# Performance work log

Measured on AMD Instinct MI355X. Metric: run time of the kernel, lower is better.

The kernel has to match this reference:

```python
import jax, jax.numpy as jnp
import numpy as np

B, N, D, H, K = 8, 128, 256, 128, 8

def setup_inputs() -> dict:
    key = jax.random.key(0)
    ks = jax.random.split(key, 6)
    E = jax.random.normal(ks[0], (B, N, D), dtype=jnp.float32)
    # kaiming_uniform-like init for linear weights
    lim1 = np.sqrt(6.0 / (2 * D))
    W1 = jax.random.uniform(ks[1], (H, 2 * D), minval=-lim1, maxval=lim1, dtype=jnp.float32)
    b1 = jnp.zeros((H,), dtype=jnp.float32)
    lim2 = np.sqrt(6.0 / H)
    W2 = jax.random.uniform(ks[2], (D, H), minval=-lim2, maxval=lim2, dtype=jnp.float32)
    b2 = jnp.zeros((D,), dtype=jnp.float32)
    q = jax.random.normal(ks[3], (K, D), dtype=jnp.float32) * (1.0 / D ** 0.5)
    return {"E": E, "W1": W1, "b1": b1, "W2": W2, "b2": b2, "q": q}

def reference(E, W1, b1, W2, b2, q):
    # phi(cat(Ei,Ej)) == relu(E_i @ W1a^T + E_j @ W1b^T + b1) @ W2^T + b2
    # Split first linear's weight to avoid materializing the [B,N,N,2D] concat.
    W1a, W1b = W1[:, :D], W1[:, D:]          # each [H, D]
    Ai = jnp.einsum('bnd,hd->bnh', E, W1a)   # [B,N,H] (row half)
    Aj = jnp.einsum('bnd,hd->bnh', E, W1b)   # [B,N,H] (col half)
    hidden = jax.nn.relu(Ai[:, :, None, :] + Aj[:, None, :, :] + b1)  # [B,N,N,H]
    # dropout is identity at inference
    # Fuse second linear with query dot: (hidden @ W2^T + b2) . q_h
    #   = hidden @ (W2^T q_h) + b2.q_h
    Wq = jnp.einsum('dh,kd->hk', W2, q)      # [H, K]
    bq = jnp.einsum('d,kd->k', b2, q)        # [K]
    logits = jnp.einsum('bijh,hk->bijh'[:0] or 'bijh,hk->bijk', hidden, Wq) + bq  # [B,N,N,K]
    M = jax.nn.sigmoid(logits).transpose(0, 3, 1, 2)  # [B,K,N,N]
    eye = jnp.eye(N, dtype=M.dtype)[None, None]
    return M * (1.0 - eye)
```

## Files before the change

kernel.cpp:

```cpp
#include <hip/hip_runtime.h>

#define PB 8
#define PN 128
#define PD 256
#define PH 128
#define PK 8
#define D2 (2*PD)

__global__ __launch_bounds__(256) void k0_prep(
        const float* __restrict__ W1, const float* __restrict__ W2,
        const float* __restrict__ b2, const float* __restrict__ q,
        float4* __restrict__ W1t4, float* __restrict__ Wq, float* __restrict__ bq)
{
    const int blk = blockIdx.x, t = threadIdx.x;
    if (blk < 64) {
        __shared__ float sm[32][33];
        const int h0 = (blk >> 4) * 32;
        const int d0 = (blk & 15) * 32;
        const int tx = t & 31, ty = t >> 5;
        #pragma unroll
        for (int r = 0; r < 4; ++r)
            sm[ty + 8 * r][tx] = W1[(h0 + ty + 8 * r) * D2 + d0 + tx];
        __syncthreads();
        const int hl = t & 31, dql = t >> 5;
        float4 w = make_float4(sm[hl][dql * 4 + 0], sm[hl][dql * 4 + 1],
                               sm[hl][dql * 4 + 2], sm[hl][dql * 4 + 3]);
        W1t4[((d0 >> 2) + dql) * PH + h0 + hl] = w;
    } else {
        __shared__ float qs[PD];
        __shared__ float red[256];
        const int k = blk - 64;
        qs[t] = q[k * PD + t];
        __syncthreads();
        if (t < PH) {
            float acc = 0.f;
            #pragma unroll 4
            for (int d = 0; d < PD; ++d)
                acc = fmaf(W2[d * PH + t], qs[d], acc);
            Wq[t * PK + k] = acc;
        }
        red[t] = b2[t] * qs[t];
        __syncthreads();
        for (int st = 128; st > 0; st >>= 1) {
            if (t < st) red[t] += red[t + st];
            __syncthreads();
        }
        if (t == 0) bq[k] = red[0];
    }
}

__global__ __launch_bounds__(256) void k1_proj(
        const float* __restrict__ E, const float* __restrict__ b1,
        const float4* __restrict__ W1t4,
        float* __restrict__ Ai, float* __restrict__ Ajt)
{
    const int blk = blockIdx.x, t = threadIdx.x;
    const int b    = blk >> 6;
    const int part = (blk >> 5) & 1;
    const int rg   = blk & 31;
    const int h    = t & (PH - 1);
    const int s    = t >> 7;
    const int n    = rg * 4 + 2 * s;

    const int ebase = __builtin_amdgcn_readfirstlane((b * PN + n) * PD);
    const float* e0 = E + ebase;
    const float* e1 = e0 + PD;
    const float4* wp = W1t4 + (part * 64) * PH + h;

    float a0 = 0.f, a1 = 0.f;
    #pragma unroll 8
    for (int dq = 0; dq < 64; ++dq) {
        const float4 w  = wp[dq * PH];
        const float4 p0 = *reinterpret_cast<const float4*>(e0 + dq * 4);
        const float4 p1 = *reinterpret_cast<const float4*>(e1 + dq * 4);
        a0 = fmaf(w.x, p0.x, a0); a0 = fmaf(w.y, p0.y, a0);
        a0 = fmaf(w.z, p0.z, a0); a0 = fmaf(w.w, p0.w, a0);
        a1 = fmaf(w.x, p1.x, a1); a1 = fmaf(w.y, p1.y, a1);
        a1 = fmaf(w.z, p1.z, a1); a1 = fmaf(w.w, p1.w, a1);
    }

    if (part == 0) {
        const float bb = b1[h];
        Ai[(b * PN + n + 0) * PH + h] = a0 + bb;
        Ai[(b * PN + n + 1) * PH + h] = a1 + bb;
    } else {
        *reinterpret_cast<float2*>(&Ajt[(b * PH + h) * PN + n]) =
            make_float2(a0, a1);
    }
}

__global__ __launch_bounds__(256) void k2_score(
        const float* __restrict__ Ai, const float* __restrict__ Ajt,
        const float4* __restrict__ Wq4, const float* __restrict__ bq,
        float* __restrict__ out)
{
    const int blk = blockIdx.x, t = threadIdx.x;
    const int b  = blk >> 5;
    const int i0 = (blk & 31) * 4;
    const int il = t >> 6;
    const int jb = t & 63;
    const int i  = i0 + il;

    const int aib = __builtin_amdgcn_readfirstlane((b * PN + i) * PH);
    const float* ai = Ai + aib;
    const float* aj = Ajt + b * PH * PN + jb;

    float acc0[PK], acc1[PK];
    const float q0 = bq[0], q1 = bq[1], q2 = bq[2], q3 = bq[3];
    const float q4 = bq[4], q5 = bq[5], q6 = bq[6], q7 = bq[7];
    acc0[0]=q0; acc0[1]=q1; acc0[2]=q2; acc0[3]=q3;
    acc0[4]=q4; acc0[5]=q5; acc0[6]=q6; acc0[7]=q7;
    acc1[0]=q0; acc1[1]=q1; acc1[2]=q2; acc1[3]=q3;
    acc1[4]=q4; acc1[5]=q5; acc1[6]=q6; acc1[7]=q7;

    #pragma unroll 8
    for (int hh = 0; hh < PH; ++hh) {
        const float a  = ai[hh];
        const float g0 = aj[hh * PN];
        const float g1 = aj[hh * PN + 64];
        const float v0 = fmaxf(a + g0, 0.f);
        const float v1 = fmaxf(a + g1, 0.f);
        const float4 wA = Wq4[hh * 2];
        const float4 wB = Wq4[hh * 2 + 1];
        acc0[0] = fmaf(v0, wA.x, acc0[0]); acc0[1] = fmaf(v0, wA.y, acc0[1]);
        acc0[2] = fmaf(v0, wA.z, acc0[2]); acc0[3] = fmaf(v0, wA.w, acc0[3]);
        acc0[4] = fmaf(v0, wB.x, acc0[4]); acc0[5] = fmaf(v0, wB.y, acc0[5]);
        acc0[6] = fmaf(v0, wB.z, acc0[6]); acc0[7] = fmaf(v0, wB.w, acc0[7]);
        acc1[0] = fmaf(v1, wA.x, acc1[0]); acc1[1] = fmaf(v1, wA.y, acc1[1]);
        acc1[2] = fmaf(v1, wA.z, acc1[2]); acc1[3] = fmaf(v1, wA.w, acc1[3]);
        acc1[4] = fmaf(v1, wB.x, acc1[4]); acc1[5] = fmaf(v1, wB.y, acc1[5]);
        acc1[6] = fmaf(v1, wB.z, acc1[6]); acc1[7] = fmaf(v1, wB.w, acc1[7]);
    }

    #pragma unroll
    for (int k = 0; k < PK; ++k) {
        float s0 = 1.f / (1.f + __expf(-acc0[k]));
        float s1 = 1.f / (1.f + __expf(-acc1[k]));
        if (jb == i)      s0 = 0.f;
        if (jb + 64 == i) s1 = 0.f;
        float* orow = out + ((b * PK + k) * PN + i) * PN;
        orow[jb]      = s0;
        orow[jb + 64] = s1;
    }
}

extern "C" void kernel_launch(void* const* d_in, const int* in_sizes, int n_in,
                              void* d_out, int out_size, void* d_ws, size_t ws_size,
                              hipStream_t stream) {
    const float* E  = (const float*)d_in[0];
    const float* W1 = (const float*)d_in[1];
    const float* b1 = (const float*)d_in[2];
    const float* W2 = (const float*)d_in[3];
    const float* b2 = (const float*)d_in[4];
    const float* q  = (const float*)d_in[5];

    float*  Ai   = (float*)d_ws;
    float*  Ajt  = Ai + PB * PN * PH;
    float4* W1t4 = (float4*)(Ajt + PB * PH * PN);
    float*  Wq   = (float*)(W1t4 + 128 * PH);
    float*  bq   = Wq + PH * PK;

    k0_prep<<<72,  256, 0, stream>>>(W1, W2, b2, q, W1t4, Wq, bq);
    k1_proj<<<512, 256, 0, stream>>>(E, b1, W1t4, Ai, Ajt);
    k2_score<<<256, 256, 0, stream>>>(Ai, Ajt, (const float4*)Wq, bq, (float*)d_out);
}
```

Before: 101.9 us.

## Split projection K-dimension across half-blocks and double score-kernel grid

In the projection kernel, each thread now computes four rows over half the D range, and the two halves of the block are combined through shared memory. This halves the serial dot-product length per thread and writes Ajt as float4. The score kernel now computes one j per thread instead of two and launches twice as many blocks, which gives more parallelism on the many-CU GPU at the cost of less reuse of the Wq and Ai loads. Both kernels add a launch_bounds minimum-blocks hint.

```diff
diff --git a/kernel.cpp b/kernel.cpp
--- a/kernel.cpp
+++ b/kernel.cpp
@@ -49,98 +49,102 @@
     }
 }
 
-__global__ __launch_bounds__(256) void k1_proj(
+__global__ __launch_bounds__(256, 2) void k1_proj(
         const float* __restrict__ E, const float* __restrict__ b1,
         const float4* __restrict__ W1t4,
         float* __restrict__ Ai, float* __restrict__ Ajt)
 {
+    __shared__ float4 psum[PH];
     const int blk = blockIdx.x, t = threadIdx.x;
     const int b    = blk >> 6;
     const int part = (blk >> 5) & 1;
     const int rg   = blk & 31;
     const int h    = t & (PH - 1);
     const int s    = t >> 7;
-    const int n    = rg * 4 + 2 * s;
+    const int n0   = rg * 4;
 
-    const int ebase = __builtin_amdgcn_readfirstlane((b * PN + n) * PD);
+    const int ebase = __builtin_amdgcn_readfirstlane((b * PN + n0) * PD + s * 128);
     const float* e0 = E + ebase;
     const float* e1 = e0 + PD;
-    const float4* wp = W1t4 + (part * 64) * PH + h;
+    const float* e2 = e1 + PD;
+    const float* e3 = e2 + PD;
+    const float4* wp = W1t4 + (part * 64 + s * 32) * PH + h;
 
-    float a0 = 0.f, a1 = 0.f;
+    float a0 = 0.f, a1 = 0.f, a2 = 0.f, a3 = 0.f;
     #pragma unroll 8
-    for (int dq = 0; dq < 64; ++dq) {
+    for (int dq = 0; dq < 32; ++dq) {
         const float4 w  = wp[dq * PH];
         const float4 p0 = *reinterpret_cast<const float4*>(e0 + dq * 4);
         const float4 p1 = *reinterpret_cast<const float4*>(e1 + dq * 4);
+        const float4 p2 = *reinterpret_cast<const float4*>(e2 + dq * 4);
+        const float4 p3 = *reinterpret_cast<const float4*>(e3 + dq * 4);
         a0 = fmaf(w.x, p0.x, a0); a0 = fmaf(w.y, p0.y, a0);
         a0 = fmaf(w.z, p0.z, a0); a0 = fmaf(w.w, p0.w, a0);
         a1 = fmaf(w.x, p1.x, a1); a1 = fmaf(w.y, p1.y, a1);
         a1 = fmaf(w.z, p1.z, a1); a1 = fmaf(w.w, p1.w, a1);
+        a2 = fmaf(w.x, p2.x, a2); a2 = fmaf(w.y, p2.y, a2);
+        a2 = fmaf(w.z, p2.z, a2); a2 = fmaf(w.w, p2.w, a2);
+        a3 = fmaf(w.x, p3.x, a3); a3 = fmaf(w.y, p3.y, a3);
+        a3 = fmaf(w.z, p3.z, a3); a3 = fmaf(w.w, p3.w, a3);
     }
 
-    if (part == 0) {
-        const float bb = b1[h];
-        Ai[(b * PN + n + 0) * PH + h] = a0 + bb;
-        Ai[(b * PN + n + 1) * PH + h] = a1 + bb;
-    } else {
-        *reinterpret_cast<float2*>(&Ajt[(b * PH + h) * PN + n]) =
-            make_float2(a0, a1);
+    if (s == 1)
+        psum[h] = make_float4(a0, a1, a2, a3);
+    __syncthreads();
+    if (s == 0) {
+        const float4 p = psum[h];
+        a0 += p.x; a1 += p.y; a2 += p.z; a3 += p.w;
+        if (part == 0) {
+            const float bb = b1[h];
+            Ai[(b * PN + n0 + 0) * PH + h] = a0 + bb;
+            Ai[(b * PN + n0 + 1) * PH + h] = a1 + bb;
+            Ai[(b * PN + n0 + 2) * PH + h] = a2 + bb;
+            Ai[(b * PN + n0 + 3) * PH + h] = a3 + bb;
+        } else {
+            *reinterpret_cast<float4*>(&Ajt[(b * PH + h) * PN + n0]) =
+                make_float4(a0, a1, a2, a3);
+        }
     }
 }
 
-__global__ __launch_bounds__(256) void k2_score(
+__global__ __launch_bounds__(256, 2) void k2_score(
         const float* __restrict__ Ai, const float* __restrict__ Ajt,
         const float4* __restrict__ Wq4, const float* __restrict__ bq,
         float* __restrict__ out)
 {
     const int blk = blockIdx.x, t = threadIdx.x;
-    const int b  = blk >> 5;
-    const int i0 = (blk & 31) * 4;
-    const int il = t >> 6;
-    const int jb = t & 63;
-    const int i  = i0 + il;
+    const int b  = blk >> 6;
+    const int ip = blk & 63;
+    const int il = t >> 7;
+    const int i  = ip * 2 + il;
+    const int j  = t & (PN - 1);
 
     const int aib = __builtin_amdgcn_readfirstlane((b * PN + i) * PH);
     const float* ai = Ai + aib;
-    const float* aj = Ajt + b * PH * PN + jb;
+    const float* aj = Ajt + b * PH * PN + j;
 
-    float acc0[PK], acc1[PK];
-    const float q0 = bq[0], q1 = bq[1], q2 = bq[2], q3 = bq[3];
-    const float q4 = bq[4], q5 = bq[5], q6 = bq[6], q7 = bq[7];
-    acc0[0]=q0; acc0[1]=q1; acc0[2]=q2; acc0[3]=q3;
-    acc0[4]=q4; acc0[5]=q5; acc0[6]=q6; acc0[7]=q7;
-    acc1[0]=q0; acc1[1]=q1; acc1[2]=q2; acc1[3]=q3;
-    acc1[4]=q4; acc1[5]=q5; acc1[6]=q6; acc1[7]=q7;
+    float acc[PK];
+    #pragma unroll
+    for (int k = 0; k < PK; ++k) acc[k] = bq[k];
 
     #pragma unroll 8
     for (int hh = 0; hh < PH; ++hh) {
-        const float a  = ai[hh];
-        const float g0 = aj[hh * PN];
-        const float g1 = aj[hh * PN + 64];
-        const float v0 = fmaxf(a + g0, 0.f);
-        const float v1 = fmaxf(a + g1, 0.f);
+        const float a = ai[hh];
+        const float g = aj[hh * PN];
+        const float v = fmaxf(a + g, 0.f);
         const float4 wA = Wq4[hh * 2];
         const float4 wB = Wq4[hh * 2 + 1];
-        acc0[0] = fmaf(v0, wA.x, acc0[0]); acc0[1] = fmaf(v0, wA.y, acc0[1]);
-        acc0[2] = fmaf(v0, wA.z, acc0[2]); acc0[3] = fmaf(v0, wA.w, acc0[3]);
-        acc0[4] = fmaf(v0, wB.x, acc0[4]); acc0[5] = fmaf(v0, wB.y, acc0[5]);
-        acc0[6] = fmaf(v0, wB.z, acc0[6]); acc0[7] = fmaf(v0, wB.w, acc0[7]);
-        acc1[0] = fmaf(v1, wA.x, acc1[0]); acc1[1] = fmaf(v1, wA.y, acc1[1]);
-        acc1[2] = fmaf(v1, wA.z, acc1[2]); acc1[3] = fmaf(v1, wA.w, acc1[3]);
-        acc1[4] = fmaf(v1, wB.x, acc1[4]); acc1[5] = fmaf(v1, wB.y, acc1[5]);
-        acc1[6] = fmaf(v1, wB.z, acc1[6]); acc1[7] = fmaf(v1, wB.w, acc1[7]);
+        acc[0] = fmaf(v, wA.x, acc[0]); acc[1] = fmaf(v, wA.y, acc[1]);
+        acc[2] = fmaf(v, wA.z, acc[2]); acc[3] = fmaf(v, wA.w, acc[3]);
+        acc[4] = fmaf(v, wB.x, acc[4]); acc[5] = fmaf(v, wB.y, acc[5]);
+        acc[6] = fmaf(v, wB.z, acc[6]); acc[7] = fmaf(v, wB.w, acc[7]);
     }
 
     #pragma unroll
     for (int k = 0; k < PK; ++k) {
-        float s0 = 1.f / (1.f + __expf(-acc0[k]));
-        float s1 = 1.f / (1.f + __expf(-acc1[k]));
-        if (jb == i)      s0 = 0.f;
-        if (jb + 64 == i) s1 = 0.f;
-        float* orow = out + ((b * PK + k) * PN + i) * PN;
-        orow[jb]      = s0;
-        orow[jb + 64] = s1;
+        float sg = 1.f / (1.f + __expf(-acc[k]));
+        if (j == i) sg = 0.f;
+        out[((b * PK + k) * PN + i) * PN + j] = sg;
     }
 }
 
@@ -162,5 +166,5 @@
 
     k0_prep<<<72,  256, 0, stream>>>(W1, W2, b2, q, W1t4, Wq, bq);
     k1_proj<<<512, 256, 0, stream>>>(E, b1, W1t4, Ai, Ajt);
-    k2_score<<<256, 256, 0, stream>>>(Ai, Ajt, (const float4*)Wq, bq, (float*)d_out);
+    k2_score<<<512, 256, 0, stream>>>(Ai, Ajt, (const float4*)Wq, bq, (float*)d_out);
 }
```

Measured after the change: 102.6 us. About the same (+0.7%).
